# Optimization experiments

Measured on AMD Instinct MI355X. Metric: run time of the kernel, lower is better.

The kernel has to match this reference:

```python
import jax, jax.numpy as jnp
import numpy as np
import math

D_MODEL = 1024
N_HEADS = 16
D_HEAD = D_MODEL // N_HEADS
MAX_SEQ_LEN = 2048
BASE = 10000.0


def _rope_tables(L):
    pos = jnp.arange(L, dtype=jnp.float32)[:, None]                      # [L,1]
    freqs = jnp.exp(-math.log(BASE) * jnp.arange(0, D_HEAD, 2, dtype=jnp.float32) / D_HEAD)  # [d/2]
    angles = pos * freqs                                                  # [L, d/2]
    return jnp.sin(angles), jnp.cos(angles)


def _apply_rope(x, sin, cos):
    # x: [B, L, H, d_head], interleaved even/odd rotation
    s = sin[None, :, None, :]
    c = cos[None, :, None, :]
    x_even, x_odd = x[..., ::2], x[..., 1::2]
    rot_even = x_even * c - x_odd * s
    rot_odd = x_even * s + x_odd * c
    # re-interleave: stack on new last axis then flatten
    return jnp.stack([rot_even, rot_odd], axis=-1).reshape(x.shape)


def setup_inputs() -> dict:
    key = jax.random.key(0)
    k0, k1, k2, k3, k4 = jax.random.split(key, 5)
    B, L = 2, 2048
    scale = 1.0 / math.sqrt(D_MODEL)
    return {
        "x": jax.random.normal(k0, (B, L, D_MODEL), dtype=jnp.float32),
        "W_q": jax.random.normal(k1, (D_MODEL, D_MODEL), dtype=jnp.float32) * scale,
        "W_k": jax.random.normal(k2, (D_MODEL, D_MODEL), dtype=jnp.float32) * scale,
        "W_v": jax.random.normal(k3, (D_MODEL, D_MODEL), dtype=jnp.float32) * scale,
        "W_o": jax.random.normal(k4, (D_MODEL, D_MODEL), dtype=jnp.float32) * scale,
    }


def reference(x, W_q, W_k, W_v, W_o):
    B, L, _ = x.shape
    sin, cos = _rope_tables(L)
    # nn.Linear(no bias): y = x @ W.T
    q = (x @ W_q.T).reshape(B, L, N_HEADS, D_HEAD)
    k = (x @ W_k.T).reshape(B, L, N_HEADS, D_HEAD)
    v = (x @ W_v.T).reshape(B, L, N_HEADS, D_HEAD)
    q = _apply_rope(q, sin, cos)
    k = _apply_rope(k, sin, cos)
    scores = jnp.einsum('blhd,bshd->bhls', q, k) / math.sqrt(D_HEAD)
    weights = jax.nn.softmax(scores, axis=-1)
    out = jnp.einsum('bhls,bshd->blhd', weights, v).reshape(B, L, D_MODEL)
    return out @ W_o.T
```

## Files before the change

kernel.cpp:

```cpp
#include <hip/hip_runtime.h>
#include <hip/hip_bf16.h>
#include <math.h>

typedef __bf16 bf16_t;
typedef __bf16 bf16x8 __attribute__((ext_vector_type(8)));
typedef __bf16 bf16x4 __attribute__((ext_vector_type(4)));
typedef float  f32x4  __attribute__((ext_vector_type(4)));
typedef float  f32x16 __attribute__((ext_vector_type(16)));
typedef unsigned u32x4 __attribute__((ext_vector_type(4)));

#define D_MODEL 1024
#define NH      16
#define DH      64
#define LSEQ    2048
#define NROWS   4096
#define LOG2E   1.44269504088896340736f
#define SHIFT_L2 17.312340490667562f

__device__ __forceinline__ void gld_lds16(bf16_t* lds, const bf16_t* g) {
  __builtin_amdgcn_global_load_lds(
      (__attribute__((address_space(1))) void*)(unsigned long long)g,
      (__attribute__((address_space(3))) void*)lds,
      16, 0, 0);
}

__device__ __forceinline__ unsigned cvtpk_bf16(float lo, float hi) {
  unsigned r;
  asm("v_cvt_pk_bf16_f32 %0, %1, %2" : "=v"(r) : "v"(lo), "v"(hi));
  return r;
}

__device__ __forceinline__ void pl32swap(unsigned& a, unsigned& b) {
  asm volatile("v_permlane32_swap_b32 %0, %1" : "+v"(a), "+v"(b));
}

__global__ __launch_bounds__(256)
void k_prep(const float* __restrict__ x,
            const float* __restrict__ w0, const float* __restrict__ w1,
            const float* __restrict__ w2, const float* __restrict__ w3,
            bf16_t* __restrict__ xb, bf16_t* __restrict__ wout, float2* __restrict__ tab)
{
  int gid = blockIdx.x * 256 + threadIdx.x;
  if (gid < 1048576) {
    float4 v = ((const float4*)x)[gid];
    bf16x4 o = { (bf16_t)v.x, (bf16_t)v.y, (bf16_t)v.z, (bf16_t)v.w };
    ((bf16x4*)xb)[gid] = o;
  } else if (gid < 2097152) {
    int i = gid - 1048576;
    int src = i >> 18;
    const float* w = (src == 0) ? w0 : (src == 1) ? w1 : (src == 2) ? w2 : w3;
    float4 v = ((const float4*)w)[i & 262143];
    bf16x4 o = { (bf16_t)v.x, (bf16_t)v.y, (bf16_t)v.z, (bf16_t)v.w };
    ((bf16x4*)wout)[i] = o;
  } else if (gid < 2162688) {
    int i = gid - 2097152;
    int l = i >> 5, p = i & 31;
    float freq = expf(-0.28782313662425575f * (float)p);
    float s, c;
    sincosf((float)l * freq, &s, &c);
    tab[i] = make_float2(c, s);
  }
}

template<int MODE>
__global__ __launch_bounds__(512, 6)
void k_gemm(const bf16_t* __restrict__ A, const bf16_t* __restrict__ B,
            int N, int K,
            float* __restrict__ Fo,
            bf16_t* __restrict__ Qo, bf16_t* __restrict__ Ko, bf16_t* __restrict__ Vo,
            const float2* __restrict__ tab)
{
  __shared__ bf16_t As[3][128 * 32];
  __shared__ bf16_t Bs[3][128 * 32];
  const int tid  = threadIdx.x;
  const int wave = tid >> 6, lane = tid & 63;
  const int hi   = lane >> 4, lo = lane & 15;

  const int bid = blockIdx.y * gridDim.x + blockIdx.x;
  const int cpx = (gridDim.x * gridDim.y) >> 3;
  const int sw  = (bid & 7) * cpx + (bid >> 3);
  const int m0  = (sw / gridDim.x) * 128;
  const int n0  = (sw % gridDim.x) * 128;

  const int wr2  = (wave >> 1) * 32, wc2 = (wave & 1) * 64;

  const int srow = tid >> 2, sslot = tid & 3;
  const bf16_t* Ap = A + (size_t)(m0 + srow) * K + (sslot ^ ((srow >> 1) & 3)) * 8;
  const bf16_t* Bp = B + (size_t)(n0 + srow) * K + (sslot ^ ((srow >> 1) & 3)) * 8;

  auto stage = [&](int buf) {
    gld_lds16(&As[buf][tid * 8], Ap);
    gld_lds16(&Bs[buf][tid * 8], Bp);
    Ap += 32; Bp += 32;
  };

  const int s16 = (hi ^ ((lo >> 1) & 3)) * 8;

  f32x4 acc[2][4] = {};

  auto compute = [&](int buf) {
    bf16x8 a[2], b[4];
    #pragma unroll
    for (int mi = 0; mi < 2; mi++)
      a[mi] = *(const bf16x8*)(&As[buf][(wr2 + mi * 16 + lo) * 32 + s16]);
    #pragma unroll
    for (int ni = 0; ni < 4; ni++)
      b[ni] = *(const bf16x8*)(&Bs[buf][(wc2 + ni * 16 + lo) * 32 + s16]);
    __builtin_amdgcn_s_setprio(1);
    #pragma unroll
    for (int mi = 0; mi < 2; mi++)
      #pragma unroll
      for (int ni = 0; ni < 4; ni++)
        acc[mi][ni] = __builtin_amdgcn_mfma_f32_16x16x32_bf16(a[mi], b[ni], acc[mi][ni], 0, 0, 0);
    __builtin_amdgcn_s_setprio(0);
  };

  const int nt = K >> 5;
  stage(0);
  stage(1);
  #pragma unroll 1
  for (int t = 0; t < nt - 2; ++t) {
    asm volatile("s_waitcnt vmcnt(2)" ::: "memory");
    __builtin_amdgcn_sched_barrier(0);
    __builtin_amdgcn_s_barrier();
    __builtin_amdgcn_sched_barrier(0);
    stage((t + 2) % 3);
    compute(t % 3);
  }
  asm volatile("s_waitcnt vmcnt(2)" ::: "memory");
  __builtin_amdgcn_sched_barrier(0);
  __builtin_amdgcn_s_barrier();
  __builtin_amdgcn_sched_barrier(0);
  compute((nt - 2) % 3);
  asm volatile("s_waitcnt vmcnt(0)" ::: "memory");
  __builtin_amdgcn_sched_barrier(0);
  __builtin_amdgcn_s_barrier();
  __builtin_amdgcn_sched_barrier(0);
  compute((nt - 1) % 3);

  if constexpr (MODE == 0) {
    #pragma unroll
    for (int mi = 0; mi < 2; mi++)
      #pragma unroll
      for (int ni = 0; ni < 4; ni++)
        #pragma unroll
        for (int r = 0; r < 4; r++) {
          int row = m0 + wr2 + mi * 16 + hi * 4 + r;
          int col = n0 + wc2 + ni * 16 + lo;
          Fo[(size_t)row * N + col] = acc[mi][ni][r];
        }
  } else {
    #pragma unroll
    for (int mi = 0; mi < 2; mi++)
      #pragma unroll
      for (int ni = 0; ni < 4; ni++)
        #pragma unroll
        for (int r = 0; r < 4; r++) {
          float val  = acc[mi][ni][r];
          float part = __shfl_xor(val, 1, 64);
          int row = m0 + wr2 + mi * 16 + hi * 4 + r;
          int col = n0 + wc2 + ni * 16 + lo;
          int which = col >> 10;
          int h = (col >> 6) & 15;
          int d = col & 63;
          int b = row >> 11, l = row & 2047;
          size_t oidx = ((size_t)(b * NH + h) * LSEQ + l) * DH + d;
          if (which == 2) {
            Vo[oidx] = (bf16_t)val;
          } else {
            float2 sc = tab[l * 32 + (d >> 1)];
            float rot = (d & 1) ? (part * sc.y + val * sc.x) : (val * sc.x - part * sc.y);
            if (which == 0) rot *= 0.125f * LOG2E;
            (which == 0 ? Qo : Ko)[oidx] = (bf16_t)rot;
          }
        }
  }
}

__global__ __launch_bounds__(512, 4)
void k_gemm_o(const bf16_t* __restrict__ A, const bf16_t* __restrict__ B,
              float* __restrict__ Fo)
{
  __shared__ bf16_t As[3][128 * 32];
  __shared__ bf16_t Bs[3][64 * 32];
  const int tid  = threadIdx.x;
  const int wave = tid >> 6, lane = tid & 63;
  const int hi   = lane >> 4, lo = lane & 15;

  const int bid = blockIdx.y * gridDim.x + blockIdx.x;
  const int cpx = (gridDim.x * gridDim.y) >> 3;
  const int sw  = (bid & 7) * cpx + (bid >> 3);
  const int m0  = (sw / gridDim.x) * 128;
  const int n0  = (sw % gridDim.x) * 64;

  const int wr2 = (wave >> 1) * 32, wc2 = (wave & 1) * 32;

  const int srow = tid >> 2, sslot = tid & 3;
  const bf16_t* Ap = A + (size_t)(m0 + srow) * 1024 + (sslot ^ ((srow >> 1) & 3)) * 8;
  const bf16_t* Bp = B + (size_t)(n0 + srow) * 1024 + (sslot ^ ((srow >> 1) & 3)) * 8;

  auto stage = [&](int buf) {
    gld_lds16(&As[buf][tid * 8], Ap);
    if (tid < 256) gld_lds16(&Bs[buf][tid * 8], Bp);
    Ap += 32; Bp += 32;
  };

  auto wait_steady = [&]() {
    if (wave < 4) { asm volatile("s_waitcnt vmcnt(2)" ::: "memory"); }
    else          { asm volatile("s_waitcnt vmcnt(1)" ::: "memory"); }
  };

  const int s16 = (hi ^ ((lo >> 1) & 3)) * 8;

  f32x4 acc[2][2] = {};

  auto compute = [&](int buf) {
    bf16x8 a[2], b[2];
    #pragma unroll
    for (int mi = 0; mi < 2; mi++)
      a[mi] = *(const bf16x8*)(&As[buf][(wr2 + mi * 16 + lo) * 32 + s16]);
    #pragma unroll
    for (int ni = 0; ni < 2; ni++)
      b[ni] = *(const bf16x8*)(&Bs[buf][(wc2 + ni * 16 + lo) * 32 + s16]);
    __builtin_amdgcn_s_setprio(1);
    #pragma unroll
    for (int mi = 0; mi < 2; mi++)
      #pragma unroll
      for (int ni = 0; ni < 2; ni++)
        acc[mi][ni] = __builtin_amdgcn_mfma_f32_16x16x32_bf16(a[mi], b[ni], acc[mi][ni], 0, 0, 0);
    __builtin_amdgcn_s_setprio(0);
  };

  stage(0);
  stage(1);
  #pragma unroll 1
  for (int t = 0; t < 30; ++t) {
    wait_steady();
    __builtin_amdgcn_sched_barrier(0);
    __builtin_amdgcn_s_barrier();
    __builtin_amdgcn_sched_barrier(0);
    stage((t + 2) % 3);
    compute(t % 3);
  }
  wait_steady();
  __builtin_amdgcn_sched_barrier(0);
  __builtin_amdgcn_s_barrier();
  __builtin_amdgcn_sched_barrier(0);
  compute(0);
  asm volatile("s_waitcnt vmcnt(0)" ::: "memory");
  __builtin_amdgcn_sched_barrier(0);
  __builtin_amdgcn_s_barrier();
  __builtin_amdgcn_sched_barrier(0);
  compute(1);

  #pragma unroll
  for (int mi = 0; mi < 2; mi++)
    #pragma unroll
    for (int ni = 0; ni < 2; ni++)
      #pragma unroll
      for (int r = 0; r < 4; r++) {
        int row = m0 + wr2 + mi * 16 + hi * 4 + r;
        int col = n0 + wc2 + ni * 16 + lo;
        Fo[(size_t)row * 1024 + col] = acc[mi][ni][r];
      }
}

__global__ __launch_bounds__(256)
void k_vt(const bf16_t* __restrict__ Vrm, bf16_t* __restrict__ VT) {
  __shared__ bf16_t T[64][66];
  const int tid = threadIdx.x;
  const int bh = blockIdx.y, l0 = blockIdx.x * 64;
  const bf16_t* src = Vrm + ((size_t)bh * LSEQ + l0) * DH;
  #pragma unroll
  for (int pass = 0; pass < 2; pass++) {
    int chunk = tid + pass * 256;
    int row = chunk >> 3, slot = chunk & 7;
    bf16x8 v = *(const bf16x8*)(src + row * DH + slot * 8);
    #pragma unroll
    for (int j = 0; j < 8; j++) T[slot * 8 + j][row] = v[j];
  }
  __syncthreads();
  bf16_t* dst = VT + (size_t)bh * DH * LSEQ + l0;
  #pragma unroll
  for (int pass = 0; pass < 2; pass++) {
    int chunk = tid + pass * 256;
    int d = chunk >> 3, slot = chunk & 7;
    bf16x8 v;
    #pragma unroll
    for (int j = 0; j < 8; j++) v[j] = T[d][slot * 8 + j];
    *(bf16x8*)(dst + (size_t)d * LSEQ + slot * 8) = v;
  }
}

__global__ __launch_bounds__(1024)
void k_attn(const bf16_t* __restrict__ Q, const bf16_t* __restrict__ K,
            const bf16_t* __restrict__ VT, bf16_t* __restrict__ O)
{
  __shared__ __align__(16) bf16_t smem[49152];
  const int tid  = threadIdx.x;
  const int wave = tid >> 6, lane = tid & 63;
  const int kg   = wave & 1;
  const int qg   = wave >> 1;
  const int ql   = lane & 31;
  const int hi   = lane >> 5;
  const int bh = blockIdx.x;
  const int qblock = blockIdx.y * 256 + qg * 32;

  bf16_t* kbase = smem + kg * 3 * 4096;
  bf16_t* vbase = smem + 24576 + kg * 3 * 4096;

  const bf16_t* Qb = Q + (size_t)bh * LSEQ * DH;

  bf16x8 qf[4];
  #pragma unroll
  for (int s = 0; s < 4; s++)
    qf[s] = *(const bf16x8*)(Qb + (size_t)(qblock + ql) * DH + s * 16 + hi * 8);

  const int r0 = qg * 8 + (lane >> 3), s0l = lane & 7;
  const int swo = (s0l ^ (r0 & 7)) * 8;
  const bf16_t* kgp = K  + ((size_t)bh * LSEQ + kg * 1024 + r0) * DH + swo;
  const bf16_t* vgp = VT + ((size_t)bh * DH + r0) * LSEQ + kg * 1024 + swo;
  const int dstoff = qg * 512 + lane * 8;

  auto stage = [&](int buf) {
    gld_lds16(kbase + buf * 4096 + dstoff, kgp);
    gld_lds16(vbase + buf * 4096 + dstoff, vgp);
    kgp += 64 * DH; vgp += 64;
  };

  f32x16 acc[2] = {};
  float lrun = 0.f;

  f32x16 shinit;
  #pragma unroll
  for (int r = 0; r < 16; r++) shinit[r] = -SHIFT_L2;

  auto compute = [&](const bf16_t* Kbuf, const bf16_t* Vbuf) {
    const char* Kcur = (const char*)Kbuf;
    f32x16 st[2] = { shinit, shinit };
    __builtin_amdgcn_s_setprio(1);
    #pragma unroll
    for (int kt = 0; kt < 2; kt++) {
      int row = kt * 32 + ql;
      int swz = (row & 7) << 4;
      #pragma unroll
      for (int s = 0; s < 4; s++) {
        bf16x8 ka = *(const bf16x8*)(Kcur + row * 128 + ((s * 32 + hi * 16) ^ swz));
        st[kt] = __builtin_amdgcn_mfma_f32_32x32x16_bf16(ka, qf[s], st[kt], 0, 0, 0);
      }
    }
    __builtin_amdgcn_s_setprio(0);

    float p[32];
    float rs = 0.f;
    #pragma unroll
    for (int kt = 0; kt < 2; kt++)
      #pragma unroll
      for (int r = 0; r < 16; r++) {
        float e = __builtin_amdgcn_exp2f(st[kt][r]);
        p[kt * 16 + r] = e;
        rs += e;
      }
    lrun += rs;

    bf16x8 pa[4];
    #pragma unroll
    for (int g = 0; g < 4; g++) {
      unsigned a0 = cvtpk_bf16(p[g * 8 + 0], p[g * 8 + 1]);
      unsigned b0 = cvtpk_bf16(p[g * 8 + 4], p[g * 8 + 5]);
      pl32swap(a0, b0);
      unsigned a1 = cvtpk_bf16(p[g * 8 + 2], p[g * 8 + 3]);
      unsigned b1 = cvtpk_bf16(p[g * 8 + 6], p[g * 8 + 7]);
      pl32swap(a1, b1);
      union { u32x4 u; bf16x8 h; } w;
      w.u[0] = a0; w.u[1] = a1; w.u[2] = b0; w.u[3] = b1;
      pa[g] = w.h;
    }

    const char* Vcur = (const char*)Vbuf;
    __builtin_amdgcn_s_setprio(1);
    #pragma unroll
    for (int dt = 0; dt < 2; dt++) {
      int row = dt * 32 + ql;
      int swz = (row & 7) << 4;
      #pragma unroll
      for (int ks = 0; ks < 4; ks++) {
        bf16x8 va = *(const bf16x8*)(Vcur + row * 128 + ((ks * 32 + hi * 16) ^ swz));
        acc[dt] = __builtin_amdgcn_mfma_f32_32x32x16_bf16(va, pa[ks], acc[dt], 0, 0, 0);
      }
    }
    __builtin_amdgcn_s_setprio(0);
  };

  stage(0);
  stage(1);
  #pragma unroll 1
  for (int t = 0; t < 14; ++t) {
    asm volatile("s_waitcnt vmcnt(2)" ::: "memory");
    __builtin_amdgcn_sched_barrier(0);
    __builtin_amdgcn_s_barrier();
    __builtin_amdgcn_sched_barrier(0);
    stage((t + 2) % 3);
    compute(kbase + (t % 3) * 4096, vbase + (t % 3) * 4096);
  }
  asm volatile("s_waitcnt vmcnt(2)" ::: "memory");
  __builtin_amdgcn_sched_barrier(0);
  __builtin_amdgcn_s_barrier();
  __builtin_amdgcn_sched_barrier(0);
  compute(kbase + 2 * 4096, vbase + 2 * 4096);
  asm volatile("s_waitcnt vmcnt(0)" ::: "memory");
  __builtin_amdgcn_sched_barrier(0);
  __builtin_amdgcn_s_barrier();
  __builtin_amdgcn_sched_barrier(0);
  compute(kbase, vbase);

  __syncthreads();
  float* xch = (float*)smem;
  float* px = xch + (qg * 64 + lane) * 34;
  if (kg == 1) {
    #pragma unroll
    for (int r = 0; r < 16; r++) { px[r] = acc[0][r]; px[16 + r] = acc[1][r]; }
    px[32] = lrun;
  }
  __syncthreads();
  if (kg == 0) {
    #pragma unroll
    for (int r = 0; r < 16; r++) { acc[0][r] += px[r]; acc[1][r] += px[16 + r]; }
    lrun += px[32];
    float lfull = lrun + __shfl_xor(lrun, 32, 64);
    float inv = 1.0f / lfull;
    const int b = bh >> 4, h = bh & 15;
    const int lpos = qblock + ql;
    #pragma unroll
    for (int dt = 0; dt < 2; dt++)
      #pragma unroll
      for (int r = 0; r < 16; r++) {
        int d = dt * 32 + (r & 3) + 8 * (r >> 2) + 4 * hi;
        O[(size_t)(b * LSEQ + lpos) * D_MODEL + h * DH + d] = (bf16_t)(acc[dt][r] * inv);
      }
  }
}

extern "C" void kernel_launch(void* const* d_in, const int* in_sizes, int n_in,
                              void* d_out, int out_size, void* d_ws, size_t ws_size,
                              hipStream_t stream)
{
  (void)in_sizes; (void)n_in; (void)out_size; (void)ws_size;
  const float* x  = (const float*)d_in[0];
  const float* Wq = (const float*)d_in[1];
  const float* Wk = (const float*)d_in[2];
  const float* Wv = (const float*)d_in[3];
  const float* Wo = (const float*)d_in[4];
  float* out = (float*)d_out;

  bf16_t* ws   = (bf16_t*)d_ws;
  bf16_t* xb   = ws;
  bf16_t* wqkv = xb + (size_t)NROWS * D_MODEL;
  bf16_t* wo   = wqkv + (size_t)3 * D_MODEL * D_MODEL;
  bf16_t* Qw   = wo + (size_t)D_MODEL * D_MODEL;
  bf16_t* Kw   = Qw + (size_t)NROWS * D_MODEL;
  bf16_t* Vw   = Kw + (size_t)NROWS * D_MODEL;
  bf16_t* VTw  = Vw + (size_t)NROWS * D_MODEL;
  bf16_t* Aw   = VTw + (size_t)NROWS * D_MODEL;
  float2* tab  = (float2*)(Aw + (size_t)NROWS * D_MODEL);

  k_prep<<<8448, 256, 0, stream>>>(x, Wq, Wk, Wv, Wo, xb, wqkv, tab);

  dim3 g1(3072 / 128, 4096 / 128);
  k_gemm<1><<<g1, 512, 0, stream>>>(xb, wqkv, 3072, 1024, nullptr, Qw, Kw, Vw, tab);

  dim3 gv(LSEQ / 64, 32);
  k_vt<<<gv, 256, 0, stream>>>(Vw, VTw);

  dim3 g2(32, LSEQ / 256);
  k_attn<<<g2, 1024, 0, stream>>>(Qw, Kw, VTw, Aw);

  dim3 g3(1024 / 64, 4096 / 128);
  k_gemm_o<<<g3, 512, 0, stream>>>(Aw, wo, out);
}
```

Before: 115.5 us.

## Fuse V transpose into QKV GEMM epilogue via shared-memory staging

The V-projection tiles of the QKV GEMM now stage their accumulators transposed in shared memory and write V directly in the [b,h,d,l] layout the attention kernel reads. This removes the separate k_vt transpose kernel, one launch, and the round trip through an intermediate row-major V buffer. The shared buffers are merged into one char array so the epilogue can reuse them. The cost is an extra block barrier and LDS traffic in the epilogue of V tiles, and the K dimension is now hardcoded to 1024.

```diff
diff --git a/kernel.cpp b/kernel.cpp
--- a/kernel.cpp
+++ b/kernel.cpp
@@ -62,19 +62,18 @@
   }
 }
 
-template<int MODE>
 __global__ __launch_bounds__(512, 6)
-void k_gemm(const bf16_t* __restrict__ A, const bf16_t* __restrict__ B,
-            int N, int K,
-            float* __restrict__ Fo,
-            bf16_t* __restrict__ Qo, bf16_t* __restrict__ Ko, bf16_t* __restrict__ Vo,
-            const float2* __restrict__ tab)
+void k_gemm_qkv(const bf16_t* __restrict__ A, const bf16_t* __restrict__ B,
+                bf16_t* __restrict__ Qo, bf16_t* __restrict__ Ko, bf16_t* __restrict__ VT,
+                const float2* __restrict__ tab)
 {
-  __shared__ bf16_t As[3][128 * 32];
-  __shared__ bf16_t Bs[3][128 * 32];
+  __shared__ __align__(16) char smem[49152];
   const int tid  = threadIdx.x;
   const int wave = tid >> 6, lane = tid & 63;
   const int hi   = lane >> 4, lo = lane & 15;
+
+  auto Asb = [&](int b) { return (bf16_t*)(smem + b * 8192); };
+  auto Bsb = [&](int b) { return (bf16_t*)(smem + 24576 + b * 8192); };
 
   const int bid = blockIdx.y * gridDim.x + blockIdx.x;
   const int cpx = (gridDim.x * gridDim.y) >> 3;
@@ -85,12 +84,12 @@
   const int wr2  = (wave >> 1) * 32, wc2 = (wave & 1) * 64;
 
   const int srow = tid >> 2, sslot = tid & 3;
-  const bf16_t* Ap = A + (size_t)(m0 + srow) * K + (sslot ^ ((srow >> 1) & 3)) * 8;
-  const bf16_t* Bp = B + (size_t)(n0 + srow) * K + (sslot ^ ((srow >> 1) & 3)) * 8;
+  const bf16_t* Ap = A + (size_t)(m0 + srow) * 1024 + (sslot ^ ((srow >> 1) & 3)) * 8;
+  const bf16_t* Bp = B + (size_t)(n0 + srow) * 1024 + (sslot ^ ((srow >> 1) & 3)) * 8;
 
   auto stage = [&](int buf) {
-    gld_lds16(&As[buf][tid * 8], Ap);
-    gld_lds16(&Bs[buf][tid * 8], Bp);
+    gld_lds16(Asb(buf) + tid * 8, Ap);
+    gld_lds16(Bsb(buf) + tid * 8, Bp);
     Ap += 32; Bp += 32;
   };
 
@@ -99,13 +98,15 @@
   f32x4 acc[2][4] = {};
 
   auto compute = [&](int buf) {
+    const bf16_t* Ac = Asb(buf);
+    const bf16_t* Bc = Bsb(buf);
     bf16x8 a[2], b[4];
     #pragma unroll
     for (int mi = 0; mi < 2; mi++)
-      a[mi] = *(const bf16x8*)(&As[buf][(wr2 + mi * 16 + lo) * 32 + s16]);
+      a[mi] = *(const bf16x8*)(Ac + (wr2 + mi * 16 + lo) * 32 + s16);
     #pragma unroll
     for (int ni = 0; ni < 4; ni++)
-      b[ni] = *(const bf16x8*)(&Bs[buf][(wc2 + ni * 16 + lo) * 32 + s16]);
+      b[ni] = *(const bf16x8*)(Bc + (wc2 + ni * 16 + lo) * 32 + s16);
     __builtin_amdgcn_s_setprio(1);
     #pragma unroll
     for (int mi = 0; mi < 2; mi++)
@@ -115,11 +116,10 @@
     __builtin_amdgcn_s_setprio(0);
   };
 
-  const int nt = K >> 5;
   stage(0);
   stage(1);
   #pragma unroll 1
-  for (int t = 0; t < nt - 2; ++t) {
+  for (int t = 0; t < 30; ++t) {
     asm volatile("s_waitcnt vmcnt(2)" ::: "memory");
     __builtin_amdgcn_sched_barrier(0);
     __builtin_amdgcn_s_barrier();
@@ -131,24 +131,38 @@
   __builtin_amdgcn_sched_barrier(0);
   __builtin_amdgcn_s_barrier();
   __builtin_amdgcn_sched_barrier(0);
-  compute((nt - 2) % 3);
+  compute(0);
   asm volatile("s_waitcnt vmcnt(0)" ::: "memory");
   __builtin_amdgcn_sched_barrier(0);
   __builtin_amdgcn_s_barrier();
   __builtin_amdgcn_sched_barrier(0);
-  compute((nt - 1) % 3);
-
-  if constexpr (MODE == 0) {
+  compute(1);
+
+  if (n0 >= 2048) {
+    __syncthreads();
+    bf16_t* T = (bf16_t*)smem;
     #pragma unroll
     for (int mi = 0; mi < 2; mi++)
       #pragma unroll
       for (int ni = 0; ni < 4; ni++)
         #pragma unroll
         for (int r = 0; r < 4; r++) {
-          int row = m0 + wr2 + mi * 16 + hi * 4 + r;
-          int col = n0 + wc2 + ni * 16 + lo;
-          Fo[(size_t)row * N + col] = acc[mi][ni][r];
+          int rl = wr2 + mi * 16 + hi * 4 + r;
+          int cl = wc2 + ni * 16 + lo;
+          T[cl * 136 + rl] = (bf16_t)acc[mi][ni][r];
         }
+    __syncthreads();
+    const int b = m0 >> 11, l0 = m0 & 2047;
+    const int hbase = (n0 - 2048) >> 6;
+    #pragma unroll
+    for (int p = 0; p < 4; p++) {
+      int chunk = tid + p * 512;
+      int cr = chunk >> 4, cs = chunk & 15;
+      bf16x8 v = *(const bf16x8*)(T + cr * 136 + cs * 8);
+      int h = hbase + (cr >> 6);
+      int d = cr & 63;
+      *(bf16x8*)(VT + ((size_t)(b * NH + h) * DH + d) * LSEQ + l0 + cs * 8) = v;
+    }
   } else {
     #pragma unroll
     for (int mi = 0; mi < 2; mi++)
@@ -165,14 +179,10 @@
           int d = col & 63;
           int b = row >> 11, l = row & 2047;
           size_t oidx = ((size_t)(b * NH + h) * LSEQ + l) * DH + d;
-          if (which == 2) {
-            Vo[oidx] = (bf16_t)val;
-          } else {
-            float2 sc = tab[l * 32 + (d >> 1)];
-            float rot = (d & 1) ? (part * sc.y + val * sc.x) : (val * sc.x - part * sc.y);
-            if (which == 0) rot *= 0.125f * LOG2E;
-            (which == 0 ? Qo : Ko)[oidx] = (bf16_t)rot;
-          }
+          float2 sc = tab[l * 32 + (d >> 1)];
+          float rot = (d & 1) ? (part * sc.y + val * sc.x) : (val * sc.x - part * sc.y);
+          if (which == 0) rot *= 0.125f * LOG2E;
+          (which == 0 ? Qo : Ko)[oidx] = (bf16_t)rot;
         }
   }
 }
@@ -263,33 +273,6 @@
         int col = n0 + wc2 + ni * 16 + lo;
         Fo[(size_t)row * 1024 + col] = acc[mi][ni][r];
       }
-}
-
-__global__ __launch_bounds__(256)
-void k_vt(const bf16_t* __restrict__ Vrm, bf16_t* __restrict__ VT) {
-  __shared__ bf16_t T[64][66];
-  const int tid = threadIdx.x;
-  const int bh = blockIdx.y, l0 = blockIdx.x * 64;
-  const bf16_t* src = Vrm + ((size_t)bh * LSEQ + l0) * DH;
-  #pragma unroll
-  for (int pass = 0; pass < 2; pass++) {
-    int chunk = tid + pass * 256;
-    int row = chunk >> 3, slot = chunk & 7;
-    bf16x8 v = *(const bf16x8*)(src + row * DH + slot * 8);
-    #pragma unroll
-    for (int j = 0; j < 8; j++) T[slot * 8 + j][row] = v[j];
-  }
-  __syncthreads();
-  bf16_t* dst = VT + (size_t)bh * DH * LSEQ + l0;
-  #pragma unroll
-  for (int pass = 0; pass < 2; pass++) {
-    int chunk = tid + pass * 256;
-    int d = chunk >> 3, slot = chunk & 7;
-    bf16x8 v;
-    #pragma unroll
-    for (int j = 0; j < 8; j++) v[j] = T[d][slot * 8 + j];
-    *(bf16x8*)(dst + (size_t)d * LSEQ + slot * 8) = v;
-  }
 }
 
 __global__ __launch_bounds__(1024)
@@ -459,18 +442,14 @@
   bf16_t* wo   = wqkv + (size_t)3 * D_MODEL * D_MODEL;
   bf16_t* Qw   = wo + (size_t)D_MODEL * D_MODEL;
   bf16_t* Kw   = Qw + (size_t)NROWS * D_MODEL;
-  bf16_t* Vw   = Kw + (size_t)NROWS * D_MODEL;
-  bf16_t* VTw  = Vw + (size_t)NROWS * D_MODEL;
+  bf16_t* VTw  = Kw + (size_t)NROWS * D_MODEL;
   bf16_t* Aw   = VTw + (size_t)NROWS * D_MODEL;
   float2* tab  = (float2*)(Aw + (size_t)NROWS * D_MODEL);
 
   k_prep<<<8448, 256, 0, stream>>>(x, Wq, Wk, Wv, Wo, xb, wqkv, tab);
 
   dim3 g1(3072 / 128, 4096 / 128);
-  k_gemm<1><<<g1, 512, 0, stream>>>(xb, wqkv, 3072, 1024, nullptr, Qw, Kw, Vw, tab);
-
-  dim3 gv(LSEQ / 64, 32);
-  k_vt<<<gv, 256, 0, stream>>>(Vw, VTw);
+  k_gemm_qkv<<<g1, 512, 0, stream>>>(xb, wqkv, Qw, Kw, VTw, tab);
 
   dim3 g2(32, LSEQ / 256);
   k_attn<<<g2, 1024, 0, stream>>>(Qw, Kw, VTw, Aw);
```

Result: faster. 108.2 us (-6.3%).
